# Kernel tuning notes

Measured on AMD Instinct MI355X. Metric: run time of the kernel, lower is better.

The kernel has to match this reference:

```python
import jax, jax.numpy as jnp
import numpy as np

N, E, HDIM, EDIM, MSG_H, UPD_H = 50000, 640000, 128, 32, 128, 128
LN_EPS = 1e-5


def setup_inputs() -> dict:
    key = jax.random.key(0)
    ks = jax.random.split(key, 12)
    def lin(k, fan_in, fan_out):
        return jax.random.normal(k, (fan_in, fan_out), dtype=jnp.float32) / np.sqrt(fan_in)
    h = jax.random.normal(ks[0], (N, HDIM), dtype=jnp.float32)
    edge_index = jax.random.randint(ks[1], (2, E), 0, N, dtype=jnp.int32)
    edge_attr = jax.random.normal(ks[2], (E, EDIM), dtype=jnp.float32)
    return {
        "h": h,
        "edge_index": edge_index,
        "edge_attr": edge_attr,
        # edge MLP: Linear(2*hdim+edim -> msg_hidden), ReLU, Linear(msg_hidden -> hdim)
        "ew1": lin(ks[3], 2 * HDIM + EDIM, MSG_H),
        "eb1": jnp.zeros((MSG_H,), jnp.float32),
        "ew2": lin(ks[4], MSG_H, HDIM),
        "eb2": jnp.zeros((HDIM,), jnp.float32),
        # node MLP: Linear(2*hdim -> upd_hidden), ReLU, Linear(upd_hidden -> hdim)
        "nw1": lin(ks[5], 2 * HDIM, UPD_H),
        "nb1": jnp.zeros((UPD_H,), jnp.float32),
        "nw2": lin(ks[6], UPD_H, HDIM),
        "nb2": jnp.zeros((HDIM,), jnp.float32),
        # LayerNorm(hdim)
        "gamma": jnp.ones((HDIM,), jnp.float32),
        "beta": jnp.zeros((HDIM,), jnp.float32),
    }


def reference(h, edge_index, edge_attr, ew1, eb1, ew2, eb2, nw1, nb1, nw2, nb2, gamma, beta):
    src, dst = edge_index[0], edge_index[1]
    # gather + concat -> edge MLP  (eval mode: dropout inactive, edge_dropout off)
    m_in = jnp.concatenate([h[src], h[dst], edge_attr], axis=1)       # [E, 2H+EDIM]
    m = jax.nn.relu(m_in @ ew1 + eb1) @ ew2 + eb2                     # [E, H]
    # scatter-add messages into destination nodes
    agg = jax.ops.segment_sum(m, dst, num_segments=h.shape[0])        # [N, H]
    # node update MLP
    u_in = jnp.concatenate([h, agg], axis=1)                          # [N, 2H]
    h_upd = jax.nn.relu(u_in @ nw1 + nb1) @ nw2 + nb2                 # [N, H]
    # residual + LayerNorm
    x = h + h_upd
    mu = jnp.mean(x, axis=-1, keepdims=True)
    var = jnp.mean(jnp.square(x - mu), axis=-1, keepdims=True)
    return (x - mu) * jax.lax.rsqrt(var + LN_EPS) * gamma + beta
```

## Files before the change

### kernel.cpp

```cpp
#include <hip/hip_runtime.h>
#include <cstdint>

#define HD 128
#define ED 32
#define BME 32
#define BMN 128
#define PAD_N 264
#define PAD_T 136
#define EGRID 512

typedef _Float16 f16;
typedef __attribute__((ext_vector_type(2))) _Float16 f16x2;
typedef __attribute__((ext_vector_type(4))) _Float16 f16x4;
typedef __attribute__((ext_vector_type(8))) _Float16 f16x8;
typedef __attribute__((ext_vector_type(4))) float    f32x4;
typedef __attribute__((ext_vector_type(4))) unsigned int u32x4;

__device__ __forceinline__ f32x4 mfma16(f16x8 a, f16x8 b, f32x4 c) {
    return __builtin_amdgcn_mfma_f32_16x16x32_f16(a, b, c, 0, 0, 0);
}
__device__ __forceinline__ f16x8 cvt8(const float* p) {
    const float4 a0 = *(const float4*)p;
    const float4 a1 = *(const float4*)(p + 4);
    f16x8 v;
    v[0] = (f16)a0.x; v[1] = (f16)a0.y; v[2] = (f16)a0.z; v[3] = (f16)a0.w;
    v[4] = (f16)a1.x; v[5] = (f16)a1.y; v[6] = (f16)a1.z; v[7] = (f16)a1.w;
    return v;
}
__device__ __forceinline__ void barrier_lds() {
    asm volatile("s_waitcnt lgkmcnt(0)" ::: "memory");
    __builtin_amdgcn_s_barrier();
    __builtin_amdgcn_sched_barrier(0);
}

__global__ __launch_bounds__(256) void zero_f32(float4* p, long n4) {
    long i = (long)blockIdx.x * blockDim.x + threadIdx.x;
    const long stride = (long)gridDim.x * blockDim.x;
    const float4 z = make_float4(0.f, 0.f, 0.f, 0.f);
    for (; i < n4; i += stride) p[i] = z;
}
__global__ __launch_bounds__(256) void zero_i32(int* p, int n) {
    int i = blockIdx.x * blockDim.x + threadIdx.x;
    if (i < n) p[i] = 0;
}
__global__ __launch_bounds__(256)
void cvt_f16_kernel(const float* __restrict__ x, f16* __restrict__ y, long n8) {
    long i = blockIdx.x * 256 + threadIdx.x;
    const long stride = (long)gridDim.x * 256;
    for (; i < n8; i += stride) *(f16x8*)(y + i * 8) = cvt8(x + i * 8);
}
__global__ __launch_bounds__(256)
void pack_all_kernel(const float* __restrict__ ew1, const float* __restrict__ ew2,
                     const float* __restrict__ nw1, const float* __restrict__ nw2,
                     f16* __restrict__ w1p, f16* __restrict__ w2p,
                     f16* __restrict__ n1p, f16* __restrict__ n2p)
{
    const int b = blockIdx.x;
    const float* w; f16* wp; int base;
    if (b < 18)      { w = ew1; wp = w1p; base = b; }
    else if (b < 26) { w = ew2; wp = w2p; base = b - 18; }
    else if (b < 42) { w = nw1; wp = n1p; base = b - 26; }
    else             { w = nw2; wp = n2p; base = b - 42; }
    const int idx = base * 256 + threadIdx.x;
    const int l  = idx & 63;
    const int fr = idx >> 6;
    const int wi = fr & 7, kt = fr >> 3;
    const int lii = l & 15, qq = l >> 4;
    const float* p = w + (size_t)(32 * kt + 8 * qq) * HD + 16 * wi + lii;
    f16x8 v;
#pragma unroll
    for (int e2 = 0; e2 < 8; ++e2) v[e2] = (f16)p[(size_t)e2 * HD];
    *(f16x8*)(wp + (size_t)idx * 8) = v;
}

__global__ __launch_bounds__(256)
void hist_kernel(const int* __restrict__ eidx, int* __restrict__ rank,
                 int* __restrict__ cnt, int E) {
    int e = blockIdx.x * 256 + threadIdx.x;
    if (e < E) rank[e] = atomicAdd(&cnt[eidx[E + e]], 1);
}
__global__ __launch_bounds__(1024)
void scan_kernel(const int* __restrict__ cnt, int* __restrict__ rs, int N) {
    __shared__ int wsum[16];
    __shared__ int s_carry;
    const int t = threadIdx.x, lane = t & 63, wid = t >> 6;
    if (t == 0) s_carry = 0;
    __syncthreads();
    for (int base = 0; base < N; base += 1024) {
        const int i = base + t;
        const int v = (i < N) ? cnt[i] : 0;
        int incl = v;
#pragma unroll
        for (int off = 1; off < 64; off <<= 1) {
            int u = __shfl_up(incl, off, 64);
            if (lane >= off) incl += u;
        }
        if (lane == 63) wsum[wid] = incl;
        __syncthreads();
        if (t == 0) {
            int s = 0;
#pragma unroll
            for (int w = 0; w < 16; ++w) { int x = wsum[w]; wsum[w] = s; s += x; }
        }
        __syncthreads();
        const int carry = s_carry;
        if (i < N) rs[i] = carry + wsum[wid] + incl - v;
        __syncthreads();
        if (t == 1023) s_carry = carry + wsum[15] + incl;
        __syncthreads();
    }
    if (threadIdx.x == 0) rs[N] = s_carry;
}
__global__ __launch_bounds__(256)
void pos_kernel(const int* __restrict__ eidx, const int* __restrict__ rs,
                int* __restrict__ pos, int E) {
    int e = blockIdx.x * 256 + threadIdx.x;
    if (e < E) pos[e] = rs[eidx[E + e]] + pos[e];
}

template <int MODE>
__global__ __launch_bounds__(256, 2)
void edge_kernel(const f16*   __restrict__ h16,
                 const int*   __restrict__ eidx,
                 const float* __restrict__ ea,
                 const f16*   __restrict__ w1p,
                 const float* __restrict__ b1,
                 const f16*   __restrict__ w2p,
                 const float* __restrict__ b2,
                 void*        __restrict__ aggm,
                 const int*   __restrict__ pos,
                 int E, int ntiles)
{
    __shared__ __align__(16) f16 sA[BME * 320];
    __shared__ __align__(16) f16 sT[BME * 128];
    __shared__ int sIdx[2][BME];

    const int t  = threadIdx.x;
    const int l  = t & 63;
    const int wv = t >> 6;
    const int li = l & 15;
    const int q  = l >> 4;
    const int lm = l & 7;
    const int r  = t >> 3;
    const int q8 = t & 7;

    f16x8 A1[2][9], A2[2][4];
#pragma unroll
    for (int ht = 0; ht < 2; ++ht) {
#pragma unroll
        for (int kt = 0; kt < 9; ++kt)
            A1[ht][kt] = *(const f16x8*)(w1p + ((size_t)(kt * 8 + wv * 2 + ht) * 64 + l) * 8);
#pragma unroll
        for (int kt = 0; kt < 4; ++kt)
            A2[ht][kt] = *(const f16x8*)(w2p + ((size_t)(kt * 8 + wv * 2 + ht) * 64 + l) * 8);
    }

    f16x8 d[4];
    f16x8 d4;
    int   psr = 0;
    auto prefetch = [&](int tile) {
        const int ec  = min(tile * BME + r, E - 1);
        const int src = eidx[ec];
        const int dst = eidx[E + ec];
        psr = (MODE == 0) ? dst : pos[ec];
        const f16* hs = h16 + (size_t)src * HD;
        const f16* hd = h16 + (size_t)dst * HD;
#pragma unroll
        for (int i = 0; i < 4; ++i) {
            const int c = (q8 + 8 * i) * 8;
            d[i] = (c < HD) ? *(const f16x8*)(hs + c)
                            : *(const f16x8*)(hd + (c - HD));
        }
        if (q8 < 4) d4 = cvt8(ea + (size_t)ec * ED + q8 * 8);
    };

    int tb = blockIdx.x;
    if (tb < ntiles) prefetch(tb);
    int par = 0;

    for (; tb < ntiles; tb += gridDim.x, par ^= 1) {
        {
            f16* row = sA + r * 320;
            const int sw = r & 7;
#pragma unroll
            for (int i = 0; i < 4; ++i) {
                const int ch = q8 + 8 * i;
                *(f16x8*)(row + ((ch ^ sw) * 8)) = d[i];
            }
            if (q8 < 4)
                *(f16x8*)(row + (((q8 + 32) ^ sw) * 8)) = d4;
            if (q8 == 0) sIdx[par][r] = psr;
        }
        barrier_lds();

        const int nt = tb + (int)gridDim.x;
        if (nt < ntiles) prefetch(nt);

        f32x4 acc[2][2];
#pragma unroll
        for (int i = 0; i < 2; ++i)
#pragma unroll
            for (int j = 0; j < 2; ++j) acc[i][j] = (f32x4){0.f, 0.f, 0.f, 0.f};
#pragma unroll
        for (int kt = 0; kt < 9; ++kt) {
#pragma unroll
            for (int e = 0; e < 2; ++e) {
                const f16x8 b = *(const f16x8*)(sA + (16 * e + li) * 320
                                                + (((4 * kt + q) ^ lm) * 8));
                acc[0][e] = mfma16(A1[0][kt], b, acc[0][e]);
                acc[1][e] = mfma16(A1[1][kt], b, acc[1][e]);
            }
        }

#pragma unroll
        for (int ht = 0; ht < 2; ++ht) {
            const int hidb = 32 * wv + 16 * ht + 4 * q;
            const float4 bb = *(const float4*)(b1 + hidb);
            const int chT = hidb >> 3;
            const int off = hidb & 7;
#pragma unroll
            for (int e = 0; e < 2; ++e) {
                const f32x4 v = acc[ht][e];
                float x0 = fmaxf(v[0] + bb.x, 0.f), x1 = fmaxf(v[1] + bb.y, 0.f);
                float x2 = fmaxf(v[2] + bb.z, 0.f), x3 = fmaxf(v[3] + bb.w, 0.f);
                f16x4 o; o[0] = (f16)x0; o[1] = (f16)x1; o[2] = (f16)x2; o[3] = (f16)x3;
                *(f16x4*)(sT + (16 * e + li) * 128 + ((chT ^ lm) * 8) + off) = o;
            }
        }
        barrier_lds();

        f32x4 acc2[2][2];
#pragma unroll
        for (int i = 0; i < 2; ++i)
#pragma unroll
            for (int j = 0; j < 2; ++j) acc2[i][j] = (f32x4){0.f, 0.f, 0.f, 0.f};
#pragma unroll
        for (int kt = 0; kt < 4; ++kt) {
#pragma unroll
            for (int e = 0; e < 2; ++e) {
                const f16x8 b = *(const f16x8*)(sT + (16 * e + li) * 128
                                                + (((4 * kt + q) ^ lm) * 8));
                acc2[0][e] = mfma16(A2[0][kt], b, acc2[0][e]);
                acc2[1][e] = mfma16(A2[1][kt], b, acc2[1][e]);
            }
        }

        if (MODE == 0) {
            float* agg = (float*)aggm;
#pragma unroll
            for (int ht = 0; ht < 2; ++ht) {
                const int hidb = 32 * wv + 16 * ht + 4 * q;
                const float4 bb = *(const float4*)(b2 + hidb);
#pragma unroll
                for (int e = 0; e < 2; ++e) {
                    const int edge = 16 * e + li;
                    if (tb * BME + edge < E) {
                        float* p = agg + (size_t)sIdx[par][edge] * HD + hidb;
                        const f32x4 v = acc2[ht][e];
                        atomicAdd(p + 0, v[0] + bb.x);
                        atomicAdd(p + 1, v[1] + bb.y);
                        atomicAdd(p + 2, v[2] + bb.z);
                        atomicAdd(p + 3, v[3] + bb.w);
                    }
                }
            }
            barrier_lds();
        } else {
            barrier_lds();
#pragma unroll
            for (int ht = 0; ht < 2; ++ht) {
                const int hidb = 32 * wv + 16 * ht + 4 * q;
                const float4 bb = *(const float4*)(b2 + hidb);
                const int chT = hidb >> 3;
                const int off = hidb & 7;
#pragma unroll
                for (int e = 0; e < 2; ++e) {
                    const f32x4 v = acc2[ht][e];
                    f16x4 o;
                    o[0] = (f16)(v[0] + bb.x); o[1] = (f16)(v[1] + bb.y);
                    o[2] = (f16)(v[2] + bb.z); o[3] = (f16)(v[3] + bb.w);
                    *(f16x4*)(sT + (16 * e + li) * 128 + ((chT ^ lm) * 8) + off) = o;
                }
            }
            barrier_lds();
            f16* m = (f16*)aggm;
#pragma unroll
            for (int i = 0; i < 2; ++i) {
                const int idx  = t + i * 256;
                const int row2 = idx >> 4;
                const int c    = idx & 15;
                if (tb * BME + row2 < E) {
                    const f16x8 v = *(const f16x8*)(sT + row2 * 128
                                                    + ((c ^ (row2 & 7)) * 8));
                    __builtin_nontemporal_store(*(const u32x4*)&v,
                        (u32x4*)(m + (size_t)sIdx[par][row2] * HD + c * 8));
                }
            }
        }
    }
}

template <int CSR>
__global__ __launch_bounds__(256, 2)
void node_kernel(const f16*   __restrict__ h16,
                 const float* __restrict__ h,
                 const f16*   __restrict__ m,
                 const int*   __restrict__ rs,
                 const float* __restrict__ aggf,
                 const f16*   __restrict__ w1p,
                 const float* __restrict__ b1,
                 const f16*   __restrict__ w2p,
                 const float* __restrict__ b2,
                 const float* __restrict__ gamma,
                 const float* __restrict__ beta,
                 float*       __restrict__ out,
                 int N)
{
    __shared__ __align__(16) f16 sA[BMN * PAD_N];
    __shared__ float sMV[2 * BMN];

    const int t  = threadIdx.x;
    const int l  = t & 63;
    const int wv = t >> 6;
    const int li = l & 15;
    const int q  = l >> 4;
    const int nbase = blockIdx.x * BMN;

    {
        const int r = t >> 1, half = t & 1;
        const int node = min(nbase + r, N - 1);
        f16* rowp = sA + r * PAD_N;
        {
            const f16* srcp = h16 + (size_t)node * HD + half * 64;
#pragma unroll
            for (int i = 0; i < 8; ++i)
                *(f16x8*)(rowp + half * 64 + i * 8) = *(const f16x8*)(srcp + i * 8);
        }
        if (CSR) {
            const int s = rs[node], en = rs[node + 1];
            float ag[64];
#pragma unroll
            for (int i = 0; i < 64; ++i) ag[i] = 0.f;
            const f16* base = m + (size_t)s * HD + half * 64;
            for (int j = 0; j < en - s; ++j) {
                const f16* rp = base + (size_t)j * HD;
#pragma unroll
                for (int i = 0; i < 8; ++i) {
                    const f16x8 v = *(const f16x8*)(rp + i * 8);
#pragma unroll
                    for (int k2 = 0; k2 < 8; ++k2) ag[i * 8 + k2] += (float)v[k2];
                }
            }
#pragma unroll
            for (int i = 0; i < 8; ++i) {
                f16x8 o;
#pragma unroll
                for (int k2 = 0; k2 < 8; ++k2) o[k2] = (f16)ag[i * 8 + k2];
                *(f16x8*)(rowp + 128 + half * 64 + i * 8) = o;
            }
        } else {
            const float* srcp = aggf + (size_t)node * HD + half * 64;
#pragma unroll
            for (int i = 0; i < 8; ++i)
                *(f16x8*)(rowp + 128 + half * 64 + i * 8) = cvt8(srcp + i * 8);
        }
    }
    __syncthreads();

    f16x8 A1[2][8];
#pragma unroll
    for (int ht = 0; ht < 2; ++ht)
#pragma unroll
        for (int kt = 0; kt < 8; ++kt)
            A1[ht][kt] = *(const f16x8*)(w1p + ((size_t)(kt * 8 + wv * 2 + ht) * 64 + l) * 8);

    f32x4 acc[2][8];
#pragma unroll
    for (int i = 0; i < 2; ++i)
#pragma unroll
        for (int j = 0; j < 8; ++j) acc[i][j] = (f32x4){0.f, 0.f, 0.f, 0.f};
#pragma unroll
    for (int kt = 0; kt < 8; ++kt) {
#pragma unroll
        for (int et = 0; et < 8; ++et) {
            const f16x8 b = *(const f16x8*)(sA + (16 * et + li) * PAD_N + 32 * kt + 8 * q);
            acc[0][et] = mfma16(A1[0][kt], b, acc[0][et]);
            acc[1][et] = mfma16(A1[1][kt], b, acc[1][et]);
        }
    }
    __syncthreads();

    f16x8 A2[2][4];
#pragma unroll
    for (int ht = 0; ht < 2; ++ht)
#pragma unroll
        for (int kt = 0; kt < 4; ++kt)
            A2[ht][kt] = *(const f16x8*)(w2p + ((size_t)(kt * 8 + wv * 2 + ht) * 64 + l) * 8);

    f16* sT = sA;
#pragma unroll
    for (int ht = 0; ht < 2; ++ht) {
        const int hidb = 32 * wv + 16 * ht + 4 * q;
        const float4 bb = *(const float4*)(b1 + hidb);
#pragma unroll
        for (int et = 0; et < 8; ++et) {
            const f32x4 v = acc[ht][et];
            float x0 = fmaxf(v[0] + bb.x, 0.f), x1 = fmaxf(v[1] + bb.y, 0.f);
            float x2 = fmaxf(v[2] + bb.z, 0.f), x3 = fmaxf(v[3] + bb.w, 0.f);
            f16x4 o; o[0] = (f16)x0; o[1] = (f16)x1; o[2] = (f16)x2; o[3] = (f16)x3;
            *(f16x4*)(sT + (16 * et + li) * PAD_T + hidb) = o;
        }
    }
    __syncthreads();

    f32x4 acc2[2][8];
#pragma unroll
    for (int i = 0; i < 2; ++i)
#pragma unroll
        for (int j = 0; j < 8; ++j) acc2[i][j] = (f32x4){0.f, 0.f, 0.f, 0.f};
#pragma unroll
    for (int kt = 0; kt < 4; ++kt) {
#pragma unroll
        for (int et = 0; et < 8; ++et) {
            const f16x8 b = *(const f16x8*)(sT + (16 * et + li) * PAD_T + 32 * kt + 8 * q);
            acc2[0][et] = mfma16(A2[0][kt], b, acc2[0][et]);
            acc2[1][et] = mfma16(A2[1][kt], b, acc2[1][et]);
        }
    }
    __syncthreads();

    float* sX = (float*)sA;
#pragma unroll
    for (int ht = 0; ht < 2; ++ht) {
        const int hidb = 32 * wv + 16 * ht + 4 * q;
        const float4 bb = *(const float4*)(b2 + hidb);
#pragma unroll
        for (int et = 0; et < 8; ++et) {
            const int node = 16 * et + li;
            const int nc   = min(nbase + node, N - 1);
            const float4 hv = *(const float4*)(h + (size_t)nc * HD + hidb);
            const f32x4 v = acc2[ht][et];
            f32x4 x;
            x[0] = v[0] + bb.x + hv.x;
            x[1] = v[1] + bb.y + hv.y;
            x[2] = v[2] + bb.z + hv.z;
            x[3] = v[3] + bb.w + hv.w;
            *(f32x4*)(sX + (size_t)node * 132 + hidb) = x;
        }
    }
    __syncthreads();

    {
        const int node  = t >> 1;
        const int half2 = t & 1;
        const float* px = sX + node * 132 + half2 * 64;
        float s = 0.f, sq = 0.f;
#pragma unroll
        for (int i = 0; i < 16; ++i) {
            const float4 v = *(const float4*)(px + i * 4);
            s  += v.x + v.y + v.z + v.w;
            sq += v.x * v.x + v.y * v.y + v.z * v.z + v.w * v.w;
        }
        s  += __shfl_xor(s, 1);
        sq += __shfl_xor(sq, 1);
        if (!half2) {
            const float mean = s * (1.f / HD);
            const float var  = sq * (1.f / HD) - mean * mean;
            sMV[node]       = mean;
            sMV[BMN + node] = rsqrtf(var + 1e-5f);
        }
    }
    __syncthreads();

#pragma unroll
    for (int i = 0; i < 16; ++i) {
        const int idx  = t + i * 256;
        const int node = idx >> 5;
        const int c4   = (idx & 31) * 4;
        if (nbase + node < N) {
            const float4 xv = *(const float4*)(sX + node * 132 + c4);
            const float4 g4 = *(const float4*)(gamma + c4);
            const float4 b4 = *(const float4*)(beta + c4);
            const float mean = sMV[node];
            const float rstd = sMV[BMN + node];
            float4 o;
            o.x = (xv.x - mean) * rstd * g4.x + b4.x;
            o.y = (xv.y - mean) * rstd * g4.y + b4.y;
            o.z = (xv.z - mean) * rstd * g4.z + b4.z;
            o.w = (xv.w - mean) * rstd * g4.w + b4.w;
            *(float4*)(out + (size_t)(nbase + node) * HD + c4) = o;
        }
    }
}

extern "C" void kernel_launch(void* const* d_in, const int* in_sizes, int n_in,
                              void* d_out, int out_size, void* d_ws, size_t ws_size,
                              hipStream_t stream)
{
    const float* h     = (const float*)d_in[0];
    const int*   eidx  = (const int*)  d_in[1];
    const float* ea    = (const float*)d_in[2];
    const float* ew1   = (const float*)d_in[3];
    const float* eb1   = (const float*)d_in[4];
    const float* ew2   = (const float*)d_in[5];
    const float* eb2   = (const float*)d_in[6];
    const float* nw1   = (const float*)d_in[7];
    const float* nb1   = (const float*)d_in[8];
    const float* nw2   = (const float*)d_in[9];
    const float* nb2   = (const float*)d_in[10];
    const float* gamma = (const float*)d_in[11];
    const float* beta  = (const float*)d_in[12];
    float* out = (float*)d_out;

    const int N = in_sizes[0] / HD;
    const int E = in_sizes[1] / 2;
    const int ntiles = (E + BME - 1) / BME;

    size_t off = 0;
    auto alloc = [&](size_t bytes) {
        size_t o = off; off += (bytes + 255) & ~(size_t)255; return o;
    };
    const size_t o_m    = alloc((size_t)E * HD * sizeof(f16));
    const size_t o_h16  = alloc((size_t)N * HD * sizeof(f16));
    const size_t o_pos  = alloc((size_t)E * sizeof(int));
    const size_t o_rs   = alloc((size_t)(N + 1) * sizeof(int));
    const size_t o_cnt  = alloc((size_t)N * sizeof(int));
    const size_t o_w1p  = alloc((size_t)9 * 8 * 64 * 8 * sizeof(f16));
    const size_t o_w2p  = alloc((size_t)4 * 8 * 64 * 8 * sizeof(f16));
    const size_t o_n1p  = alloc((size_t)8 * 8 * 64 * 8 * sizeof(f16));
    const size_t o_n2p  = alloc((size_t)4 * 8 * 64 * 8 * sizeof(f16));
    const bool csr = (off <= ws_size);
    char* ws = (char*)d_ws;

    if (csr) {
        f16* mb   = (f16*)(ws + o_m);
        f16* h16  = (f16*)(ws + o_h16);
        int* pos  = (int*)(ws + o_pos);
        int* rs   = (int*)(ws + o_rs);
        int* cnt  = (int*)(ws + o_cnt);
        f16* w1p  = (f16*)(ws + o_w1p);
        f16* w2p  = (f16*)(ws + o_w2p);
        f16* n1p  = (f16*)(ws + o_n1p);
        f16* n2p  = (f16*)(ws + o_n2p);

        zero_i32<<<(N + 255) / 256, 256, 0, stream>>>(cnt, N);
        hist_kernel<<<(E + 255) / 256, 256, 0, stream>>>(eidx, pos, cnt, E);
        scan_kernel<<<1, 1024, 0, stream>>>(cnt, rs, N);
        pos_kernel<<<(E + 255) / 256, 256, 0, stream>>>(eidx, rs, pos, E);
        cvt_f16_kernel<<<2048, 256, 0, stream>>>(h, h16, (long)N * HD / 8);
        pack_all_kernel<<<50, 256, 0, stream>>>(ew1, ew2, nw1, nw2, w1p, w2p, n1p, n2p);
        edge_kernel<1><<<EGRID, 256, 0, stream>>>(
            h16, eidx, ea, w1p, eb1, w2p, eb2, (void*)mb, pos, E, ntiles);
        node_kernel<1><<<(N + BMN - 1) / BMN, 256, 0, stream>>>(
            h16, h, mb, rs, nullptr, n1p, nb1, n2p, nb2, gamma, beta, out, N);
    } else {
        size_t foff = 0;
        auto falloc = [&](size_t bytes) {
            size_t o = foff; foff += (bytes + 255) & ~(size_t)255; return o;
        };
        float* agg = (float*)(ws + falloc((size_t)N * HD * sizeof(float)));
        f16*   h16 = (f16*)  (ws + falloc((size_t)N * HD * sizeof(f16)));
        f16*   w1p = (f16*)  (ws + falloc((size_t)9 * 8 * 64 * 8 * sizeof(f16)));
        f16*   w2p = (f16*)  (ws + falloc((size_t)4 * 8 * 64 * 8 * sizeof(f16)));
        f16*   n1p = (f16*)  (ws + falloc((size_t)8 * 8 * 64 * 8 * sizeof(f16)));
        f16*   n2p = (f16*)  (ws + falloc((size_t)4 * 8 * 64 * 8 * sizeof(f16)));

        zero_f32<<<1024, 256, 0, stream>>>((float4*)agg, (long)N * HD / 4);
        cvt_f16_kernel<<<2048, 256, 0, stream>>>(h, h16, (long)N * HD / 8);
        pack_all_kernel<<<50, 256, 0, stream>>>(ew1, ew2, nw1, nw2, w1p, w2p, n1p, n2p);
        edge_kernel<0><<<EGRID, 256, 0, stream>>>(
            h16, eidx, ea, w1p, eb1, w2p, eb2, (void*)agg, nullptr, E, ntiles);
        node_kernel<0><<<(N + BMN - 1) / BMN, 256, 0, stream>>>(
            h16, h, nullptr, nullptr, agg, n1p, nb1, n2p, nb2, gamma, beta, out, N);
    }
}
```

Baseline: 265.7 us.

## Process edges in CSR order via inverse permutation for contiguous message writes

Adds an inverse-permutation kernel mapping each CSR slot to its original edge. The edge kernel then iterates over slots, gathering src/dst and edge_attr through that map, and writes messages contiguously instead of scattering each row to pos[e]. This trades scattered 256-byte stores for an extra indirection and more random edge_attr reads, plus one more small kernel launch. Processing edges grouped by destination may also improve locality of the h[dst] gathers.

```diff
diff --git a/kernel.cpp b/kernel.cpp
--- a/kernel.cpp
+++ b/kernel.cpp
@@ -117,6 +117,11 @@
     int e = blockIdx.x * 256 + threadIdx.x;
     if (e < E) pos[e] = rs[eidx[E + e]] + pos[e];
 }
+__global__ __launch_bounds__(256)
+void inv_kernel(const int* __restrict__ pos, int* __restrict__ inv, int E) {
+    int e = blockIdx.x * 256 + threadIdx.x;
+    if (e < E) inv[pos[e]] = e;
+}
 
 template <int MODE>
 __global__ __launch_bounds__(256, 2)
@@ -128,7 +133,7 @@
                  const f16*   __restrict__ w2p,
                  const float* __restrict__ b2,
                  void*        __restrict__ aggm,
-                 const int*   __restrict__ pos,
+                 const int*   __restrict__ inv,
                  int E, int ntiles)
 {
     __shared__ __align__(16) f16 sA[BME * 320];
@@ -159,10 +164,13 @@
     f16x8 d4;
     int   psr = 0;
     auto prefetch = [&](int tile) {
-        const int ec  = min(tile * BME + r, E - 1);
-        const int src = eidx[ec];
-        const int dst = eidx[E + ec];
-        psr = (MODE == 0) ? dst : pos[ec];
+        const int slot = min(tile * BME + r, E - 1);
+        int e;
+        if (MODE == 0) e = slot;
+        else           e = inv[slot];
+        const int src = eidx[e];
+        const int dst = eidx[E + e];
+        if (MODE == 0) psr = dst;
         const f16* hs = h16 + (size_t)src * HD;
         const f16* hd = h16 + (size_t)dst * HD;
 #pragma unroll
@@ -171,7 +179,7 @@
             d[i] = (c < HD) ? *(const f16x8*)(hs + c)
                             : *(const f16x8*)(hd + (c - HD));
         }
-        if (q8 < 4) d4 = cvt8(ea + (size_t)ec * ED + q8 * 8);
+        if (q8 < 4) d4 = cvt8(ea + (size_t)e * ED + q8 * 8);
     };
 
     int tb = blockIdx.x;
@@ -189,7 +197,7 @@
             }
             if (q8 < 4)
                 *(f16x8*)(row + (((q8 + 32) ^ sw) * 8)) = d4;
-            if (q8 == 0) sIdx[par][r] = psr;
+            if (MODE == 0 && q8 == 0) sIdx[par][r] = psr;
         }
         barrier_lds();
 
@@ -284,6 +292,7 @@
             }
             barrier_lds();
             f16* m = (f16*)aggm;
+            const size_t mbase = (size_t)tb * BME * HD;
 #pragma unroll
             for (int i = 0; i < 2; ++i) {
                 const int idx  = t + i * 256;
@@ -293,7 +302,7 @@
                     const f16x8 v = *(const f16x8*)(sT + row2 * 128
                                                     + ((c ^ (row2 & 7)) * 8));
                     __builtin_nontemporal_store(*(const u32x4*)&v,
-                        (u32x4*)(m + (size_t)sIdx[par][row2] * HD + c * 8));
+                        (u32x4*)(m + mbase + (size_t)row2 * HD + c * 8));
                 }
             }
         }
@@ -523,6 +532,7 @@
     const size_t o_m    = alloc((size_t)E * HD * sizeof(f16));
     const size_t o_h16  = alloc((size_t)N * HD * sizeof(f16));
     const size_t o_pos  = alloc((size_t)E * sizeof(int));
+    const size_t o_inv  = alloc((size_t)E * sizeof(int));
     const size_t o_rs   = alloc((size_t)(N + 1) * sizeof(int));
     const size_t o_cnt  = alloc((size_t)N * sizeof(int));
     const size_t o_w1p  = alloc((size_t)9 * 8 * 64 * 8 * sizeof(f16));
@@ -536,6 +546,7 @@
         f16* mb   = (f16*)(ws + o_m);
         f16* h16  = (f16*)(ws + o_h16);
         int* pos  = (int*)(ws + o_pos);
+        int* inv  = (int*)(ws + o_inv);
         int* rs   = (int*)(ws + o_rs);
         int* cnt  = (int*)(ws + o_cnt);
         f16* w1p  = (f16*)(ws + o_w1p);
@@ -547,10 +558,11 @@
         hist_kernel<<<(E + 255) / 256, 256, 0, stream>>>(eidx, pos, cnt, E);
         scan_kernel<<<1, 1024, 0, stream>>>(cnt, rs, N);
         pos_kernel<<<(E + 255) / 256, 256, 0, stream>>>(eidx, rs, pos, E);
+        inv_kernel<<<(E + 255) / 256, 256, 0, stream>>>(pos, inv, E);
         cvt_f16_kernel<<<2048, 256, 0, stream>>>(h, h16, (long)N * HD / 8);
         pack_all_kernel<<<50, 256, 0, stream>>>(ew1, ew2, nw1, nw2, w1p, w2p, n1p, n2p);
         edge_kernel<1><<<EGRID, 256, 0, stream>>>(
-            h16, eidx, ea, w1p, eb1, w2p, eb2, (void*)mb, pos, E, ntiles);
+            h16, eidx, ea, w1p, eb1, w2p, eb2, (void*)mb, inv, E, ntiles);
         node_kernel<1><<<(N + BMN - 1) / BMN, 256, 0, stream>>>(
             h16, h, mb, rs, nullptr, n1p, nb1, n2p, nb2, gamma, beta, out, N);
     } else {
```

After: 283.2 us. 6.6% more time.
